# Kernel tuning notes

Measured on AMD Instinct MI355X. Metric: run time of the kernel, lower is better.

The kernel has to match this reference:

```python
import jax, jax.numpy as jnp
import numpy as np

B, N, IN_F, OUT_F, H = 4, 2048, 256, 256, 8
NH = OUT_F // H  # 32
SLOPE = 0.2
NEG_INF = -9e15


def setup_inputs() -> dict:
    key = jax.random.key(0)
    k1, k2, k3, k4 = jax.random.split(key, 4)
    h = jax.random.normal(k1, (B, N, IN_F), jnp.float32)
    adj = jax.random.randint(k2, (B, N, N), 0, 2).astype(jnp.int32)
    # xavier_uniform with gain 1.414
    gw = 1.414 * np.sqrt(6.0 / (IN_F + H * NH))
    W = jax.random.uniform(k3, (IN_F, H * NH), jnp.float32, -gw, gw)
    ga = 1.414 * np.sqrt(6.0 / (2 * NH + 1))
    a = jax.random.uniform(k4, (2 * NH, 1), jnp.float32, -ga, ga)
    return {"h": h, "adj": adj, "W": W, "a": a}


def reference(h, adj, W, a):
    Wh = h @ W                              # [B, N, H*NH]
    # Faithful to torch .view: raw memory reinterpretation, not a transpose.
    Wh = Wh.reshape(B, H, N, NH)            # [B, H, N, NH]
    Wh1 = Wh @ a[:NH]                       # [B, H, N, 1]
    Wh2 = Wh @ a[NH:]                       # [B, H, N, 1]
    e = Wh1 + jnp.swapaxes(Wh2, 2, 3)       # [B, H, N, N] additive scores
    e = jnp.where(e >= 0, e, SLOPE * e)     # leaky relu
    e = jnp.where(adj[:, None] > 0, e, NEG_INF)
    attn = jax.nn.softmax(e, axis=-1)       # [B, H, N, N]
    h_prime = attn @ Wh                     # [B, H, N, NH]
    h_prime = h_prime.reshape(B, N, OUT_F)  # raw reshape, matches torch .view
    return jax.nn.elu(h_prime)
```

## Files before the change

### kernel.cpp

```cpp
#include <hip/hip_runtime.h>
#include <hip/hip_bf16.h>

#define B_    4
#define N_    2048
#define INF_  256
#define OUTF_ 256
#define H_    8
#define NH_   32
#define BH_   (B_ * H_)
#define ROWS_ (B_ * N_)
#define VSZ_  (N_ * NH_)

typedef float  f32x4 __attribute__((ext_vector_type(4)));
typedef short  s16x8 __attribute__((ext_vector_type(8)));

__global__ __launch_bounds__(256) void gemm_wh(const float* __restrict__ A,
                                               const float* __restrict__ Wm,
                                               float* __restrict__ C) {
    __shared__ float As[16][68];
    __shared__ float Bs[16][68];
    const int tid = threadIdx.x;
    const int bm = blockIdx.x * 64;
    const int bn = blockIdx.y * 64;
    const int tm = (tid >> 4) << 2;
    const int tn = (tid & 15) << 2;
    const int ar = tid >> 2, ac = (tid & 3) << 2;
    const int br = tid >> 4, bc = (tid & 15) << 2;
    float acc[4][4] = {};

    for (int k0 = 0; k0 < 256; k0 += 16) {
        float4 av = *(const float4*)(A + (size_t)(bm + ar) * 256 + k0 + ac);
        float4 bv = *(const float4*)(Wm + (size_t)(k0 + br) * 256 + bn + bc);
        As[ac + 0][ar] = av.x;
        As[ac + 1][ar] = av.y;
        As[ac + 2][ar] = av.z;
        As[ac + 3][ar] = av.w;
        *(float4*)&Bs[br][bc] = bv;
        __syncthreads();
#pragma unroll
        for (int kk = 0; kk < 16; ++kk) {
            float a4[4], b4[4];
            *(float4*)a4 = *(const float4*)&As[kk][tm];
            *(float4*)b4 = *(const float4*)&Bs[kk][tn];
#pragma unroll
            for (int i = 0; i < 4; ++i)
#pragma unroll
                for (int j = 0; j < 4; ++j)
                    acc[i][j] = fmaf(a4[i], b4[j], acc[i][j]);
        }
        __syncthreads();
    }
#pragma unroll
    for (int i = 0; i < 4; ++i)
        *(float4*)(C + (size_t)(bm + tm + i) * 256 + bn + tn) = *(float4*)acc[i];
}

__global__ __launch_bounds__(256) void st_kernel(const float* __restrict__ Wh,
                                                 const float* __restrict__ a,
                                                 float* __restrict__ s,
                                                 float* __restrict__ t) {
    const int row = blockIdx.x * 256 + threadIdx.x;
    const float* v = Wh + (size_t)row * NH_;
    float s_ = 0.f, t_ = 0.f;
#pragma unroll
    for (int k = 0; k < NH_; k += 4) {
        float4 vv = *(const float4*)(v + k);
        float4 a1 = *(const float4*)(a + k);
        float4 a2 = *(const float4*)(a + NH_ + k);
        s_ += vv.x * a1.x + vv.y * a1.y + vv.z * a1.z + vv.w * a1.w;
        t_ += vv.x * a2.x + vv.y * a2.y + vv.z * a2.z + vv.w * a2.w;
    }
    s[row] = s_;
    t[row] = t_;
}

__global__ __launch_bounds__(256) void bitpack(const int* __restrict__ adj,
                                               unsigned int* __restrict__ adjw) {
    const int idx = blockIdx.x * 256 + threadIdx.x;
    const int4* p = (const int4*)(adj + (size_t)idx * 32);
    unsigned int w = 0;
#pragma unroll
    for (int q = 0; q < 8; ++q) {
        int4 v = p[q];
        w |= (v.x != 0 ? 1u : 0u) << (q * 4 + 0);
        w |= (v.y != 0 ? 1u : 0u) << (q * 4 + 1);
        w |= (v.z != 0 ? 1u : 0u) << (q * 4 + 2);
        w |= (v.w != 0 ? 1u : 0u) << (q * 4 + 3);
    }
    adjw[idx] = w;
}

__global__ __launch_bounds__(256) void attn_kernel(const float* __restrict__ Wh,
                                                   const float* __restrict__ s,
                                                   const float* __restrict__ t,
                                                   const unsigned int* __restrict__ adjw,
                                                   float* __restrict__ out) {
    const int bh = blockIdx.y;
    const int b  = bh >> 3;
    const int i0 = blockIdx.x * 64;
    const int tid = threadIdx.x;
    const int wv = tid >> 6;
    const int l  = tid & 63;
    const int lr = l & 15;
    const int lg = l >> 4;

    __shared__ int   adjL[64][65];
    __shared__ short Bf[2][2][64][8];

    {
        const int4* ab = (const int4*)(adjw + (size_t)(b * N_ + i0) * 64);
#pragma unroll
        for (int k = 0; k < 4; ++k) {
            int idx4 = tid + k * 256;
            int4 v = ab[idx4];
            int row = idx4 >> 4, w0 = (idx4 << 2) & 63;
            adjL[row][w0 + 0] = v.x;
            adjL[row][w0 + 1] = v.y;
            adjL[row][w0 + 2] = v.z;
            adjL[row][w0 + 3] = v.w;
        }
    }

    const float* Vbase = Wh + (size_t)bh * VSZ_;
    const float* tB    = t + (size_t)bh * N_;
    const float  sreg  = s[(size_t)bh * N_ + i0 + wv * 16 + lr];

    const int sj  = tid >> 3;
    const int sf0 = (tid & 7) << 2;
    const int si  = sj & 7, skg = sj >> 3;

    auto stage = [&](int jt, int bb) {
        float4 v = *(const float4*)(Vbase + (size_t)(jt * 32 + sj) * NH_ + sf0);
        float pv4[4] = {v.x, v.y, v.z, v.w};
#pragma unroll
        for (int q = 0; q < 4; ++q) {
            int f = sf0 + q;
            int nt = f >> 4, li = skg * 16 + (f & 15);
            unsigned u = __float_as_uint(pv4[q]);
            Bf[bb][nt][li][si] = (short)((u + 0x8000u) >> 16);
        }
    };

    stage(0, 0);
    __syncthreads();

    f32x4 acc0 = {0.f, 0.f, 0.f, 0.f};
    f32x4 acc1 = {0.f, 0.f, 0.f, 0.f};
    float rs = 0.f;

    for (int jt = 0; jt < 64; ++jt) {
        const int cur = jt & 1;
        if (jt < 63) stage(jt + 1, cur ^ 1);

        const unsigned word = (unsigned)adjL[wv * 16 + lr][jt];
        const unsigned wsh  = word >> (lg * 8);
        const float* tp = tB + jt * 32 + lg * 8;
        float4 t0 = *(const float4*)tp;
        float4 t1 = *(const float4*)(tp + 4);
        float tv[8] = {t0.x, t0.y, t0.z, t0.w, t1.x, t1.y, t1.z, t1.w};
        s16x8 af;
#pragma unroll
        for (int i = 0; i < 8; ++i) {
            float x = sreg + tv[i];
            float e = fmaxf(x, 0.2f * x);
            float pv = __expf(e);
            pv = (wsh & (1u << i)) ? pv : 0.0f;
            unsigned pb = (__float_as_uint(pv) + 0x8000u) >> 16;
            af[i] = (short)pb;
            rs += __uint_as_float(pb << 16);
        }

        s16x8 b0 = *(const s16x8*)(&Bf[cur][0][l][0]);
        s16x8 b1 = *(const s16x8*)(&Bf[cur][1][l][0]);
        acc0 = __builtin_amdgcn_mfma_f32_16x16x32_bf16(af, b0, acc0, 0, 0, 0);
        acc1 = __builtin_amdgcn_mfma_f32_16x16x32_bf16(af, b1, acc1, 0, 0, 0);
        __syncthreads();
    }

    rs += __shfl_xor(rs, 16);
    rs += __shfl_xor(rs, 32);
    const float inv = 1.0f / rs;

    float* obase = out + (size_t)bh * VSZ_;
#pragma unroll
    for (int r = 0; r < 4; ++r) {
        const int rloc = 4 * lg + r;
        const float ir = __shfl(inv, (l & 48) + rloc);
        const int row = i0 + wv * 16 + rloc;
        float v0 = acc0[r] * ir;
        float v1 = acc1[r] * ir;
        v0 = v0 > 0.f ? v0 : expm1f(v0);
        v1 = v1 > 0.f ? v1 : expm1f(v1);
        obase[(size_t)row * NH_ + lr]      = v0;
        obase[(size_t)row * NH_ + 16 + lr] = v1;
    }
}

extern "C" void kernel_launch(void* const* d_in, const int* in_sizes, int n_in,
                              void* d_out, int out_size, void* d_ws, size_t ws_size,
                              hipStream_t stream) {
    const float* h   = (const float*)d_in[0];
    const int*   adj = (const int*)d_in[1];
    const float* W   = (const float*)d_in[2];
    const float* a   = (const float*)d_in[3];
    float* out = (float*)d_out;

    char* ws = (char*)d_ws;
    float* Wh = (float*)ws;
    float* s  = (float*)(ws + (size_t)ROWS_ * OUTF_ * 4);
    float* t  = (float*)(ws + (size_t)ROWS_ * OUTF_ * 4 + BH_ * N_ * 4);
    unsigned int* adjw = (unsigned int*)(ws + (size_t)ROWS_ * OUTF_ * 4 + 2 * BH_ * N_ * 4);

    gemm_wh<<<dim3(ROWS_ / 64, OUTF_ / 64), 256, 0, stream>>>(h, W, Wh);
    st_kernel<<<(BH_ * N_) / 256, 256, 0, stream>>>(Wh, a, s, t);
    bitpack<<<(B_ * N_ * (N_ / 32)) / 256, 256, 0, stream>>>(adj, adjw);
    attn_kernel<<<dim3(N_ / 64, BH_), 256, 0, stream>>>(Wh, s, t, adjw, out);
}
```

Baseline: 178.9 us.

## Pre-pack V into MFMA-ready bf16 fragments and drop per-tile barriers

Adds a vconv kernel that converts Wh to bf16 already arranged in the per-lane MFMA B-operand layout. The attention kernel can then load each lane's fragment straight from global memory with register prefetch, instead of staging through shared memory with a __syncthreads every tile. It also caches the whole t vector for the head in LDS and splits the row-sum accumulation into two chains. The cost is an extra kernel launch and an extra global write and read of V in bf16. V rounding now uses round-to-nearest-even in place of round-half-up.

```diff
diff --git a/kernel.cpp b/kernel.cpp
--- a/kernel.cpp
+++ b/kernel.cpp
@@ -74,6 +74,25 @@
     t[row] = t_;
 }
 
+__global__ __launch_bounds__(256) void vconv(const float* __restrict__ Wh,
+                                             short* __restrict__ Vb) {
+    const int t = blockIdx.x * 256 + threadIdx.x;
+    const int lane = t & 63;
+    const int nt   = (t >> 6) & 1;
+    const int jt   = (t >> 7) & 63;
+    const int bh   = t >> 13;
+    const float* src = Wh + (size_t)bh * VSZ_ +
+                       (size_t)(jt * 32 + (lane >> 4) * 8) * NH_ +
+                       nt * 16 + (lane & 15);
+    s16x8 v;
+#pragma unroll
+    for (int i = 0; i < 8; ++i) {
+        unsigned u = __float_as_uint(src[(size_t)i * NH_]);
+        v[i] = (short)((u + 0x7fffu + ((u >> 16) & 1u)) >> 16);
+    }
+    *(s16x8*)(Vb + (size_t)t * 8) = v;
+}
+
 __global__ __launch_bounds__(256) void bitpack(const int* __restrict__ adj,
                                                unsigned int* __restrict__ adjw) {
     const int idx = blockIdx.x * 256 + threadIdx.x;
@@ -90,7 +109,7 @@
     adjw[idx] = w;
 }
 
-__global__ __launch_bounds__(256) void attn_kernel(const float* __restrict__ Wh,
+__global__ __launch_bounds__(256) void attn_kernel(const short* __restrict__ Vb,
                                                    const float* __restrict__ s,
                                                    const float* __restrict__ t,
                                                    const unsigned int* __restrict__ adjw,
@@ -104,8 +123,8 @@
     const int lr = l & 15;
     const int lg = l >> 4;
 
-    __shared__ int   adjL[64][65];
-    __shared__ short Bf[2][2][64][8];
+    __shared__ int   adjL[64][68];
+    __shared__ float ts[2048];
 
     {
         const int4* ab = (const int4*)(adjw + (size_t)(b * N_ + i0) * 64);
@@ -113,70 +132,58 @@
         for (int k = 0; k < 4; ++k) {
             int idx4 = tid + k * 256;
             int4 v = ab[idx4];
-            int row = idx4 >> 4, w0 = (idx4 << 2) & 63;
-            adjL[row][w0 + 0] = v.x;
-            adjL[row][w0 + 1] = v.y;
-            adjL[row][w0 + 2] = v.z;
-            adjL[row][w0 + 3] = v.w;
-        }
-    }
-
-    const float* Vbase = Wh + (size_t)bh * VSZ_;
-    const float* tB    = t + (size_t)bh * N_;
-    const float  sreg  = s[(size_t)bh * N_ + i0 + wv * 16 + lr];
-
-    const int sj  = tid >> 3;
-    const int sf0 = (tid & 7) << 2;
-    const int si  = sj & 7, skg = sj >> 3;
-
-    auto stage = [&](int jt, int bb) {
-        float4 v = *(const float4*)(Vbase + (size_t)(jt * 32 + sj) * NH_ + sf0);
-        float pv4[4] = {v.x, v.y, v.z, v.w};
-#pragma unroll
-        for (int q = 0; q < 4; ++q) {
-            int f = sf0 + q;
-            int nt = f >> 4, li = skg * 16 + (f & 15);
-            unsigned u = __float_as_uint(pv4[q]);
-            Bf[bb][nt][li][si] = (short)((u + 0x8000u) >> 16);
-        }
-    };
-
-    stage(0, 0);
+            *(int4*)&adjL[idx4 >> 4][(idx4 << 2) & 63] = v;
+        }
+    }
+    {
+        const float4* tsrc = (const float4*)(t + (size_t)bh * N_);
+        float4 v0 = tsrc[tid];
+        float4 v1 = tsrc[tid + 256];
+        *(float4*)&ts[tid * 4] = v0;
+        *(float4*)&ts[1024 + tid * 4] = v1;
+    }
+    const float sreg = s[(size_t)bh * N_ + i0 + wv * 16 + lr];
     __syncthreads();
 
+    const s16x8* vb = (const s16x8*)(Vb + (size_t)bh * 65536);
+
+    s16x8 nb0 = vb[l];
+    s16x8 nb1 = vb[64 + l];
     f32x4 acc0 = {0.f, 0.f, 0.f, 0.f};
     f32x4 acc1 = {0.f, 0.f, 0.f, 0.f};
-    float rs = 0.f;
+    float rs0 = 0.f, rs1 = 0.f;
 
     for (int jt = 0; jt < 64; ++jt) {
-        const int cur = jt & 1;
-        if (jt < 63) stage(jt + 1, cur ^ 1);
-
-        const unsigned word = (unsigned)adjL[wv * 16 + lr][jt];
-        const unsigned wsh  = word >> (lg * 8);
-        const float* tp = tB + jt * 32 + lg * 8;
-        float4 t0 = *(const float4*)tp;
-        float4 t1 = *(const float4*)(tp + 4);
-        float tv[8] = {t0.x, t0.y, t0.z, t0.w, t1.x, t1.y, t1.z, t1.w};
-        s16x8 af;
+        s16x8 b0 = nb0, b1 = nb1;
+        if (jt < 63) {
+            nb0 = vb[(jt + 1) * 128 + l];
+            nb1 = vb[(jt + 1) * 128 + 64 + l];
+        }
+        const unsigned wsh = ((unsigned)adjL[wv * 16 + lr][jt]) >> (lg * 8);
+        float tv[8];
+        *(float4*)&tv[0] = *(const float4*)&ts[jt * 32 + lg * 8];
+        *(float4*)&tv[4] = *(const float4*)&ts[jt * 32 + lg * 8 + 4];
+        float p[8];
 #pragma unroll
         for (int i = 0; i < 8; ++i) {
             float x = sreg + tv[i];
             float e = fmaxf(x, 0.2f * x);
             float pv = __expf(e);
-            pv = (wsh & (1u << i)) ? pv : 0.0f;
-            unsigned pb = (__float_as_uint(pv) + 0x8000u) >> 16;
-            af[i] = (short)pb;
-            rs += __uint_as_float(pb << 16);
-        }
-
-        s16x8 b0 = *(const s16x8*)(&Bf[cur][0][l][0]);
-        s16x8 b1 = *(const s16x8*)(&Bf[cur][1][l][0]);
+            p[i] = (wsh & (1u << i)) ? pv : 0.f;
+        }
+        rs0 += p[0] + p[2] + p[4] + p[6];
+        rs1 += p[1] + p[3] + p[5] + p[7];
+        s16x8 af;
+#pragma unroll
+        for (int i = 0; i < 8; ++i) {
+            unsigned u = __float_as_uint(p[i]);
+            af[i] = (short)((u + 0x8000u) >> 16);
+        }
         acc0 = __builtin_amdgcn_mfma_f32_16x16x32_bf16(af, b0, acc0, 0, 0, 0);
         acc1 = __builtin_amdgcn_mfma_f32_16x16x32_bf16(af, b1, acc1, 0, 0, 0);
-        __syncthreads();
-    }
-
+    }
+
+    float rs = rs0 + rs1;
     rs += __shfl_xor(rs, 16);
     rs += __shfl_xor(rs, 32);
     const float inv = 1.0f / rs;
@@ -207,12 +214,15 @@
 
     char* ws = (char*)d_ws;
     float* Wh = (float*)ws;
-    float* s  = (float*)(ws + (size_t)ROWS_ * OUTF_ * 4);
-    float* t  = (float*)(ws + (size_t)ROWS_ * OUTF_ * 4 + BH_ * N_ * 4);
-    unsigned int* adjw = (unsigned int*)(ws + (size_t)ROWS_ * OUTF_ * 4 + 2 * BH_ * N_ * 4);
+    char*  p1 = ws + (size_t)ROWS_ * OUTF_ * 4;
+    float* s  = (float*)p1;
+    float* t  = (float*)(p1 + BH_ * N_ * 4);
+    unsigned int* adjw = (unsigned int*)(p1 + 2 * BH_ * N_ * 4);
+    short* Vb = (short*)(p1 + 2 * BH_ * N_ * 4 + (size_t)B_ * N_ * 64 * 4);
 
     gemm_wh<<<dim3(ROWS_ / 64, OUTF_ / 64), 256, 0, stream>>>(h, W, Wh);
     st_kernel<<<(BH_ * N_) / 256, 256, 0, stream>>>(Wh, a, s, t);
+    vconv<<<(BH_ * N_ * NH_ / 8) / 256, 256, 0, stream>>>(Wh, Vb);
     bitpack<<<(B_ * N_ * (N_ / 32)) / 256, 256, 0, stream>>>(adj, adjw);
-    attn_kernel<<<dim3(N_ / 64, BH_), 256, 0, stream>>>(Wh, s, t, adjw, out);
-}
+    attn_kernel<<<dim3(N_ / 64, BH_), 256, 0, stream>>>(Vb, s, t, adjw, out);
+}
```

Result: faster. 175.1 us (-2.1%).
